# Kernel optimization log

Measured on AMD Instinct MI355X. Metric: run time of the kernel, lower is better.

The kernel has to match this reference:

```python
import jax, jax.numpy as jnp
import numpy as np

B, N, D = 64, 2048, 128  # batch, neighbors, embedding_dim (= region_dim)


def setup_inputs() -> dict:
    key = jax.random.key(0)
    ks = jax.random.split(key, 8)
    inv_sqrt_d = 1.0 / np.sqrt(D).astype(np.float32)
    return {
        "e_i": jax.random.normal(ks[0], (B, D), jnp.float32),
        "e_j": jax.random.normal(ks[1], (B, N, D), jnp.float32),
        "imp_j": jax.random.uniform(ks[2], (B, N), jnp.float32),
        "R_lk": jax.random.normal(ks[3], (D, D), jnp.float32),
        "W_q": jax.random.normal(ks[4], (D, D), jnp.float32) * inv_sqrt_d,
        "W_k": jax.random.normal(ks[5], (D, D), jnp.float32) * inv_sqrt_d,
        "W_v": jax.random.normal(ks[6], (D, D), jnp.float32) * inv_sqrt_d,
        "omega": jax.random.normal(ks[7], (D,), jnp.float32),
    }


def reference(e_i, e_j, imp_j, R_lk, W_q, W_k, W_v, omega):
    # torch nn.Linear(x) = x @ W.T; weights are [out, in] = [D, D]
    q = e_i @ W_q.T                                   # [B, D]
    k = jnp.einsum('bnd,ed->bne', e_j, W_k)           # [B, N, D]
    # additive tanh attention score sigma_ij = tanh(q_i + k_j) . omega
    sigma = jnp.tanh(q[:, None, :] + k) @ omega       # [B, N]
    exp_s = jnp.exp(sigma)
    denom = jnp.sum(exp_s, axis=1, keepdims=True) + 1e-9
    a = imp_j * exp_s / denom                         # [B, N]  (a_ij, squeezed)
    v = jnp.einsum('bnd,ed->bne', e_j, W_v)           # [B, N, D]
    # A_i_t = sum_n a_ij * v_j  (identical math to A_i_l in the source)
    A_l = jnp.einsum('bn,bnd->bd', a, v)              # [B, D]
    # sum_n R[l,k] * a[b,n] * v[b,n,k] = R[l,k] * A_l[b,k]  -- fused, no [B,N,D,D]
    A_lk = R_lk[None, :, :] * A_l[:, None, :]         # [B, D, D]
    return A_l, A_lk, A_l
```

## Files before the change

kernel.cpp:

```cpp
#include <hip/hip_runtime.h>
#include <stdint.h>

#define BB 64
#define NN 2048
#define DD 128
#define ROWS 64
#define CPB 2

typedef __attribute__((ext_vector_type(8))) short short8;
typedef __attribute__((ext_vector_type(4))) float f32x4;

__device__ __forceinline__ unsigned short f2bf_rtne(float x) {
    union { float f; unsigned int u; } v; v.f = x;
    unsigned int r = v.u + 0x7fffu + ((v.u >> 16) & 1u);
    return (unsigned short)(r >> 16);
}
__device__ __forceinline__ float bf2f(unsigned short h) {
    union { unsigned int u; float f; } v; v.u = ((unsigned int)h) << 16;
    return v.f;
}
__device__ __forceinline__ float tanh_fast(float x) {
    float ax = fabsf(x);
    float e  = __expf(-2.f * ax);
    float t  = (1.f - e) / (1.f + e);
    return copysignf(t, x);
}

__global__ __launch_bounds__(256) void aegis_prep(
    const float* __restrict__ e_i, const float* __restrict__ Wq,
    const float* __restrict__ Wk,
    float* __restrict__ qbuf, unsigned short* __restrict__ Bhig,
    unsigned short* __restrict__ Blog,
    float* __restrict__ sprime, float* __restrict__ denom)
{
    __shared__ float eis[DD];
    const int t = threadIdx.x, blk = blockIdx.x;
    if (blk < 8) {
        const int tid = blk * 256 + t;
        const int lr = tid & 15, lg = (tid >> 4) & 3, ks = (tid >> 6) & 3, et = tid >> 8;
        const int e = et * 16 + lr, k = ks * 32 + lg * 8;
        const float* src = Wk + e * DD + k;
        float4 x0 = *reinterpret_cast<const float4*>(src);
        float4 x1 = *reinterpret_cast<const float4*>(src + 4);
        float xs[8] = {x0.x, x0.y, x0.z, x0.w, x1.x, x1.y, x1.z, x1.w};
        short8 h, l;
        #pragma unroll
        for (int j = 0; j < 8; ++j) {
            unsigned short hb = f2bf_rtne(xs[j]);
            float rem = xs[j] - bf2f(hb);
            h[j] = (short)hb;
            l[j] = (short)f2bf_rtne(rem);
        }
        *reinterpret_cast<short8*>(Bhig + (size_t)tid * 8) = h;
        *reinterpret_cast<short8*>(Blog + (size_t)tid * 8) = l;
    } else {
        const int b = blk - 8;
        if (t < DD) eis[t] = e_i[b * DD + t];
        __syncthreads();
        if (t < DD) {
            float acc = 0.f;
            const float4* wr = reinterpret_cast<const float4*>(Wq + t * DD);
            const float4* ev = reinterpret_cast<const float4*>(eis);
            #pragma unroll 8
            for (int i = 0; i < 32; ++i) {
                float4 w = wr[i], e = ev[i];
                acc = fmaf(w.x, e.x, acc); acc = fmaf(w.y, e.y, acc);
                acc = fmaf(w.z, e.z, acc); acc = fmaf(w.w, e.w, acc);
            }
            qbuf[b * DD + t] = acc;
            sprime[b * DD + t] = 0.f;
        }
        if (t == 0) denom[b] = 0.f;
    }
}

__global__ __launch_bounds__(256, 4) void aegis_main(
    const float* __restrict__ e_j, const float* __restrict__ imp,
    const float* __restrict__ omega, const float* __restrict__ qbuf,
    const unsigned short* __restrict__ Bhig, const unsigned short* __restrict__ Blog,
    float* __restrict__ sprime, float* __restrict__ denom)
{
    __shared__ unsigned short Ehi[ROWS * DD];
    __shared__ unsigned short Elo[ROWS * DD];
    __shared__ float sig[ROWS][4];
    __shared__ float wrow[ROWS];
    __shared__ float scol[DD];

    const int t    = threadIdx.x;
    const int b    = blockIdx.x >> 4;
    const int cb   = blockIdx.x & 15;
    const int lane = t & 63;
    const int w    = t >> 6;
    const int lr   = lane & 15;
    const int lg   = lane >> 4;

    short8 Bh[2][4], Bl[2][4];
    #pragma unroll
    for (int ct = 0; ct < 2; ++ct)
        #pragma unroll
        for (int ks = 0; ks < 4; ++ks) {
            const int fi = (((2 * w + ct) * 4 + ks) * 4 + lg) * 16 + lr;
            Bh[ct][ks] = *reinterpret_cast<const short8*>(Bhig + (size_t)fi * 8);
            Bl[ct][ks] = *reinterpret_cast<const short8*>(Blog + (size_t)fi * 8);
        }

    float qv[2], ov[2];
    #pragma unroll
    for (int ct = 0; ct < 2; ++ct) {
        const int c = 32 * w + 16 * ct + lr;
        qv[ct] = qbuf[b * DD + c];
        ov[ct] = omega[c];
    }

    const int d  = t & 127;
    const int hf = t >> 7;
    float sacc = 0.f, den_local = 0.f;

    #pragma unroll 1
    for (int c = 0; c < CPB; ++c) {
        const int row0 = (cb * CPB + c) * ROWS;
        __syncthreads();

        {
            const float4* src = reinterpret_cast<const float4*>(
                e_j + ((size_t)(b * NN + row0)) * DD);
            #pragma unroll
            for (int i = 0; i < 8; ++i) {
                const int idx = t + i * 256;
                const int rr  = idx >> 5;
                const int bc  = (idx & 31) * 8;
                float4 v = src[idx];
                float xs[4] = {v.x, v.y, v.z, v.w};
                unsigned short hs[4], ls[4];
                #pragma unroll
                for (int j = 0; j < 4; ++j) {
                    hs[j] = f2bf_rtne(xs[j]);
                    ls[j] = f2bf_rtne(xs[j] - bf2f(hs[j]));
                }
                uint2 ph, pl;
                ph.x = (unsigned)hs[0] | ((unsigned)hs[1] << 16);
                ph.y = (unsigned)hs[2] | ((unsigned)hs[3] << 16);
                pl.x = (unsigned)ls[0] | ((unsigned)ls[1] << 16);
                pl.y = (unsigned)ls[2] | ((unsigned)ls[3] << 16);
                const int off = rr * 256 + (bc ^ ((rr & 7) << 4));
                *reinterpret_cast<uint2*>(reinterpret_cast<char*>(Ehi) + off) = ph;
                *reinterpret_cast<uint2*>(reinterpret_cast<char*>(Elo) + off) = pl;
            }
        }
        __syncthreads();

        #pragma unroll 1
        for (int rt = 0; rt < 4; ++rt) {
            f32x4 a0 = {0.f, 0.f, 0.f, 0.f};
            f32x4 a1 = {0.f, 0.f, 0.f, 0.f};
            const int arow = rt * 16 + lr;
            const int rbase = arow * 256;
            const int rsw   = (lr & 7) << 4;
            #pragma unroll
            for (int ks = 0; ks < 4; ++ks) {
                const int off = rbase + ((ks * 64 + lg * 16) ^ rsw);
                short8 ah = *reinterpret_cast<const short8*>(
                    reinterpret_cast<const char*>(Ehi) + off);
                short8 al = *reinterpret_cast<const short8*>(
                    reinterpret_cast<const char*>(Elo) + off);
                a0 = __builtin_amdgcn_mfma_f32_16x16x32_bf16(ah, Bh[0][ks], a0, 0, 0, 0);
                a1 = __builtin_amdgcn_mfma_f32_16x16x32_bf16(ah, Bh[1][ks], a1, 0, 0, 0);
                a0 = __builtin_amdgcn_mfma_f32_16x16x32_bf16(ah, Bl[0][ks], a0, 0, 0, 0);
                a1 = __builtin_amdgcn_mfma_f32_16x16x32_bf16(ah, Bl[1][ks], a1, 0, 0, 0);
                a0 = __builtin_amdgcn_mfma_f32_16x16x32_bf16(al, Bh[0][ks], a0, 0, 0, 0);
                a1 = __builtin_amdgcn_mfma_f32_16x16x32_bf16(al, Bh[1][ks], a1, 0, 0, 0);
            }
            float sp[4];
            #pragma unroll
            for (int i = 0; i < 4; ++i) {
                float x0 = qv[0] + a0[i];
                float x1 = qv[1] + a1[i];
                sp[i] = fmaf(ov[0], tanh_fast(x0), ov[1] * tanh_fast(x1));
            }
            #pragma unroll
            for (int m = 1; m < 16; m <<= 1) {
                #pragma unroll
                for (int i = 0; i < 4; ++i) sp[i] += __shfl_xor(sp[i], m);
            }
            if (lr == 0) {
                #pragma unroll
                for (int i = 0; i < 4; ++i) sig[rt * 16 + 4 * lg + i][w] = sp[i];
            }
        }
        __syncthreads();

        if (t < ROWS) {
            float sg = sig[t][0] + sig[t][1] + sig[t][2] + sig[t][3];
            float es = __expf(sg);
            wrow[t]  = es * imp[b * NN + row0 + t];
            float ds = es;
            #pragma unroll
            for (int m = 1; m < 64; m <<= 1) ds += __shfl_xor(ds, m);
            if (t == 0) den_local += ds;
        }
        __syncthreads();

        {
            float part = 0.f;
            #pragma unroll
            for (int rr = hf * 32; rr < hf * 32 + 32; ++rr) {
                const int off = rr * 256 + ((2 * d) ^ ((rr & 7) << 4));
                float ev = bf2f(*reinterpret_cast<const unsigned short*>(
                               reinterpret_cast<const char*>(Ehi) + off))
                         + bf2f(*reinterpret_cast<const unsigned short*>(
                               reinterpret_cast<const char*>(Elo) + off));
                part = fmaf(wrow[rr], ev, part);
            }
            sacc += part;
        }
    }

    if (hf == 0) scol[d] = sacc;
    __syncthreads();
    if (hf == 1) atomicAdd(&sprime[b * DD + d], sacc + scol[d]);
    if (t == 0) atomicAdd(&denom[b], den_local);
}

__global__ __launch_bounds__(256) void aegis_epi(
    const float* __restrict__ sprime, const float* __restrict__ denomv,
    const float* __restrict__ Wv, const float* __restrict__ R,
    float* __restrict__ out)
{
    __shared__ float sn[DD];
    __shared__ float alred[DD][2];
    __shared__ float al[DD];
    const int t = threadIdx.x, b = blockIdx.x;

    if (t < DD) sn[t] = sprime[b * DD + t] / (denomv[b] + 1e-9f);
    __syncthreads();
    {
        const int l = t >> 1, h = t & 1;
        const float4* wr = reinterpret_cast<const float4*>(Wv + l * DD + h * 64);
        const float4* sv = reinterpret_cast<const float4*>(sn + h * 64);
        float acc = 0.f;
        #pragma unroll 8
        for (int i = 0; i < 16; ++i) {
            float4 w = wr[i], e = sv[i];
            acc = fmaf(w.x, e.x, acc); acc = fmaf(w.y, e.y, acc);
            acc = fmaf(w.z, e.z, acc); acc = fmaf(w.w, e.w, acc);
        }
        alred[l][h] = acc;
    }
    __syncthreads();
    if (t < DD) {
        float v = alred[t][0] + alred[t][1];
        al[t] = v;
        out[b * DD + t] = v;
        out[8192 + 1048576 + b * DD + t] = v;
    }
    __syncthreads();
    float4* dst = reinterpret_cast<float4*>(out + 8192 + (size_t)b * DD * DD);
    const float4* rsrc = reinterpret_cast<const float4*>(R);
    #pragma unroll
    for (int i = 0; i < 16; ++i) {
        const int idx = t + i * 256;
        float4 r = rsrc[idx];
        const int k0 = (idx & 31) * 4;
        float4 o;
        o.x = r.x * al[k0];     o.y = r.y * al[k0 + 1];
        o.z = r.z * al[k0 + 2]; o.w = r.w * al[k0 + 3];
        dst[idx] = o;
    }
}

extern "C" void kernel_launch(void* const* d_in, const int* in_sizes, int n_in,
                              void* d_out, int out_size, void* d_ws, size_t ws_size,
                              hipStream_t stream) {
    const float* e_i = (const float*)d_in[0];
    const float* e_j = (const float*)d_in[1];
    const float* imp = (const float*)d_in[2];
    const float* R   = (const float*)d_in[3];
    const float* Wq  = (const float*)d_in[4];
    const float* Wk  = (const float*)d_in[5];
    const float* Wv  = (const float*)d_in[6];
    const float* om  = (const float*)d_in[7];

    float* out    = (float*)d_out;
    float* sprime = (float*)d_ws;
    float* denom  = (float*)((char*)d_ws + 32768);

    float* qbuf = out + 8192;
    unsigned short* Bhig = (unsigned short*)(out + 8192 + 8192);
    unsigned short* Blog = Bhig + 16384;

    aegis_prep<<<dim3(72), dim3(256), 0, stream>>>(
        e_i, Wq, Wk, qbuf, Bhig, Blog, sprime, denom);
    aegis_main<<<dim3(BB * 16), dim3(256), 0, stream>>>(
        e_j, imp, om, qbuf, Bhig, Blog, sprime, denom);
    aegis_epi<<<dim3(BB), dim3(256), 0, stream>>>(sprime, denom, Wv, R, out);
}
```

Before: 159.4 us.

## Prefetch next e_j chunk into registers and restructure weighted-sum reduction in main kernel

The main kernel now loads both 64-row chunks of e_j into registers up front. The second chunk's global load is issued before the first chunk's MFMA score phase, so the memory latency overlaps compute. The weighted column sum is reworked so each thread reads packed pairs of bf16 values across 16 rows and partial sums are combined through shared memory. Barriers become a custom LDS-wait plus s_barrier. Occupancy is lowered from 4 to 3 blocks per CU to make room for the extra registers held by the prefetch buffer.

```diff
diff --git a/kernel.cpp b/kernel.cpp
--- a/kernel.cpp
+++ b/kernel.cpp
@@ -24,6 +24,10 @@
     float e  = __expf(-2.f * ax);
     float t  = (1.f - e) / (1.f + e);
     return copysignf(t, x);
+}
+__device__ __forceinline__ void ldsbar() {
+    asm volatile("s_waitcnt lgkmcnt(0)" ::: "memory");
+    __builtin_amdgcn_s_barrier();
 }
 
 __global__ __launch_bounds__(256) void aegis_prep(
@@ -74,7 +78,7 @@
     }
 }
 
-__global__ __launch_bounds__(256, 4) void aegis_main(
+__global__ __launch_bounds__(256, 3) void aegis_main(
     const float* __restrict__ e_j, const float* __restrict__ imp,
     const float* __restrict__ omega, const float* __restrict__ qbuf,
     const unsigned short* __restrict__ Bhig, const unsigned short* __restrict__ Blog,
@@ -84,7 +88,7 @@
     __shared__ unsigned short Elo[ROWS * DD];
     __shared__ float sig[ROWS][4];
     __shared__ float wrow[ROWS];
-    __shared__ float scol[DD];
+    __shared__ float scolq[4][DD];
 
     const int t    = threadIdx.x;
     const int b    = blockIdx.x >> 4;
@@ -93,6 +97,13 @@
     const int w    = t >> 6;
     const int lr   = lane & 15;
     const int lg   = lane >> 4;
+    const int row0 = cb * (CPB * ROWS);
+
+    float4 st[8];
+    const float4* ejp = reinterpret_cast<const float4*>(
+        e_j + (size_t)(b * NN + row0) * DD);
+    #pragma unroll
+    for (int i = 0; i < 8; ++i) st[i] = ejp[t + i * 256];
 
     short8 Bh[2][4], Bl[2][4];
     #pragma unroll
@@ -111,26 +122,125 @@
         qv[ct] = qbuf[b * DD + c];
         ov[ct] = omega[c];
     }
-
-    const int d  = t & 127;
-    const int hf = t >> 7;
+    float impv[CPB];
+    if (t < ROWS) {
+        #pragma unroll
+        for (int c = 0; c < CPB; ++c) impv[c] = imp[b * NN + row0 + c * ROWS + t];
+    }
+
+    #pragma unroll
+    for (int i = 0; i < 8; ++i) {
+        const int idx = t + i * 256;
+        const int rr  = idx >> 5;
+        const int bc  = (idx & 31) * 8;
+        float xs[4] = {st[i].x, st[i].y, st[i].z, st[i].w};
+        unsigned short hs[4], ls[4];
+        #pragma unroll
+        for (int j = 0; j < 4; ++j) {
+            hs[j] = f2bf_rtne(xs[j]);
+            ls[j] = f2bf_rtne(xs[j] - bf2f(hs[j]));
+        }
+        uint2 ph, pl;
+        ph.x = (unsigned)hs[0] | ((unsigned)hs[1] << 16);
+        ph.y = (unsigned)hs[2] | ((unsigned)hs[3] << 16);
+        pl.x = (unsigned)ls[0] | ((unsigned)ls[1] << 16);
+        pl.y = (unsigned)ls[2] | ((unsigned)ls[3] << 16);
+        const int off = rr * 256 + (bc ^ ((rr & 7) << 4));
+        *reinterpret_cast<uint2*>(reinterpret_cast<char*>(Ehi) + off) = ph;
+        *reinterpret_cast<uint2*>(reinterpret_cast<char*>(Elo) + off) = pl;
+    }
+    #pragma unroll
+    for (int i = 0; i < 8; ++i) st[i] = ejp[2048 + t + i * 256];
+
+    ldsbar();
+
     float sacc = 0.f, den_local = 0.f;
-
-    #pragma unroll 1
+    const int rq = t >> 6;
+    const int cp = t & 63;
+
+    #pragma unroll
     for (int c = 0; c < CPB; ++c) {
-        const int row0 = (cb * CPB + c) * ROWS;
-        __syncthreads();
+        #pragma unroll 1
+        for (int rt = 0; rt < 4; ++rt) {
+            f32x4 a0 = {0.f, 0.f, 0.f, 0.f};
+            f32x4 a1 = {0.f, 0.f, 0.f, 0.f};
+            const int arow  = rt * 16 + lr;
+            const int rbase = arow * 256;
+            const int rsw   = (lr & 7) << 4;
+            #pragma unroll
+            for (int ks = 0; ks < 4; ++ks) {
+                const int off = rbase + ((ks * 64 + lg * 16) ^ rsw);
+                short8 ah = *reinterpret_cast<const short8*>(
+                    reinterpret_cast<const char*>(Ehi) + off);
+                short8 al = *reinterpret_cast<const short8*>(
+                    reinterpret_cast<const char*>(Elo) + off);
+                a0 = __builtin_amdgcn_mfma_f32_16x16x32_bf16(ah, Bh[0][ks], a0, 0, 0, 0);
+                a1 = __builtin_amdgcn_mfma_f32_16x16x32_bf16(ah, Bh[1][ks], a1, 0, 0, 0);
+                a0 = __builtin_amdgcn_mfma_f32_16x16x32_bf16(ah, Bl[0][ks], a0, 0, 0, 0);
+                a1 = __builtin_amdgcn_mfma_f32_16x16x32_bf16(ah, Bl[1][ks], a1, 0, 0, 0);
+                a0 = __builtin_amdgcn_mfma_f32_16x16x32_bf16(al, Bh[0][ks], a0, 0, 0, 0);
+                a1 = __builtin_amdgcn_mfma_f32_16x16x32_bf16(al, Bh[1][ks], a1, 0, 0, 0);
+            }
+            float sp[4];
+            #pragma unroll
+            for (int i = 0; i < 4; ++i) {
+                float x0 = qv[0] + a0[i];
+                float x1 = qv[1] + a1[i];
+                sp[i] = fmaf(ov[0], tanh_fast(x0), ov[1] * tanh_fast(x1));
+            }
+            #pragma unroll
+            for (int m = 1; m < 16; m <<= 1) {
+                #pragma unroll
+                for (int i = 0; i < 4; ++i) sp[i] += __shfl_xor(sp[i], m);
+            }
+            if (lr == 0) {
+                #pragma unroll
+                for (int i = 0; i < 4; ++i) sig[rt * 16 + 4 * lg + i][w] = sp[i];
+            }
+        }
+        ldsbar();
+
+        if (t < ROWS) {
+            float sg = sig[t][0] + sig[t][1] + sig[t][2] + sig[t][3];
+            float es = __expf(sg);
+            wrow[t]  = es * impv[c];
+            float ds = es;
+            #pragma unroll
+            for (int m = 1; m < 64; m <<= 1) ds += __shfl_xor(ds, m);
+            if (t == 0) den_local += ds;
+        }
+        ldsbar();
 
         {
-            const float4* src = reinterpret_cast<const float4*>(
-                e_j + ((size_t)(b * NN + row0)) * DD);
+            float a0 = 0.f, a1 = 0.f;
+            #pragma unroll
+            for (int j = 0; j < 16; ++j) {
+                const int rr  = rq * 16 + j;
+                const int off = rr * 256 + ((4 * cp) ^ ((rr & 7) << 4));
+                const unsigned hbits = *reinterpret_cast<const unsigned*>(
+                    reinterpret_cast<const char*>(Ehi) + off);
+                const unsigned lbits = *reinterpret_cast<const unsigned*>(
+                    reinterpret_cast<const char*>(Elo) + off);
+                const float wv = wrow[rr];
+                float v0 = bf2f((unsigned short)hbits) + bf2f((unsigned short)lbits);
+                float v1 = bf2f((unsigned short)(hbits >> 16)) + bf2f((unsigned short)(lbits >> 16));
+                a0 = fmaf(wv, v0, a0);
+                a1 = fmaf(wv, v1, a1);
+            }
+            scolq[rq][2 * cp]     = a0;
+            scolq[rq][2 * cp + 1] = a1;
+        }
+        ldsbar();
+
+        if (t < DD) sacc += scolq[0][t] + scolq[1][t] + scolq[2][t] + scolq[3][t];
+
+        if (c + 1 < CPB) {
             #pragma unroll
             for (int i = 0; i < 8; ++i) {
                 const int idx = t + i * 256;
                 const int rr  = idx >> 5;
                 const int bc  = (idx & 31) * 8;
-                float4 v = src[idx];
-                float xs[4] = {v.x, v.y, v.z, v.w};
+                float xs[4] = {st[i].x, st[i].y, st[i].z, st[i].w};
                 unsigned short hs[4], ls[4];
                 #pragma unroll
                 for (int j = 0; j < 4; ++j) {
@@ -146,78 +256,11 @@
                 *reinterpret_cast<uint2*>(reinterpret_cast<char*>(Ehi) + off) = ph;
                 *reinterpret_cast<uint2*>(reinterpret_cast<char*>(Elo) + off) = pl;
             }
-        }
-        __syncthreads();
-
-        #pragma unroll 1
-        for (int rt = 0; rt < 4; ++rt) {
-            f32x4 a0 = {0.f, 0.f, 0.f, 0.f};
-            f32x4 a1 = {0.f, 0.f, 0.f, 0.f};
-            const int arow = rt * 16 + lr;
-            const int rbase = arow * 256;
-            const int rsw   = (lr & 7) << 4;
-            #pragma unroll
-            for (int ks = 0; ks < 4; ++ks) {
-                const int off = rbase + ((ks * 64 + lg * 16) ^ rsw);
-                short8 ah = *reinterpret_cast<const short8*>(
-                    reinterpret_cast<const char*>(Ehi) + off);
-                short8 al = *reinterpret_cast<const short8*>(
-                    reinterpret_cast<const char*>(Elo) + off);
-                a0 = __builtin_amdgcn_mfma_f32_16x16x32_bf16(ah, Bh[0][ks], a0, 0, 0, 0);
-                a1 = __builtin_amdgcn_mfma_f32_16x16x32_bf16(ah, Bh[1][ks], a1, 0, 0, 0);
-                a0 = __builtin_amdgcn_mfma_f32_16x16x32_bf16(ah, Bl[0][ks], a0, 0, 0, 0);
-                a1 = __builtin_amdgcn_mfma_f32_16x16x32_bf16(ah, Bl[1][ks], a1, 0, 0, 0);
-                a0 = __builtin_amdgcn_mfma_f32_16x16x32_bf16(al, Bh[0][ks], a0, 0, 0, 0);
-                a1 = __builtin_amdgcn_mfma_f32_16x16x32_bf16(al, Bh[1][ks], a1, 0, 0, 0);
-            }
-            float sp[4];
-            #pragma unroll
-            for (int i = 0; i < 4; ++i) {
-                float x0 = qv[0] + a0[i];
-                float x1 = qv[1] + a1[i];
-                sp[i] = fmaf(ov[0], tanh_fast(x0), ov[1] * tanh_fast(x1));
-            }
-            #pragma unroll
-            for (int m = 1; m < 16; m <<= 1) {
-                #pragma unroll
-                for (int i = 0; i < 4; ++i) sp[i] += __shfl_xor(sp[i], m);
-            }
-            if (lr == 0) {
-                #pragma unroll
-                for (int i = 0; i < 4; ++i) sig[rt * 16 + 4 * lg + i][w] = sp[i];
-            }
-        }
-        __syncthreads();
-
-        if (t < ROWS) {
-            float sg = sig[t][0] + sig[t][1] + sig[t][2] + sig[t][3];
-            float es = __expf(sg);
-            wrow[t]  = es * imp[b * NN + row0 + t];
-            float ds = es;
-            #pragma unroll
-            for (int m = 1; m < 64; m <<= 1) ds += __shfl_xor(ds, m);
-            if (t == 0) den_local += ds;
-        }
-        __syncthreads();
-
-        {
-            float part = 0.f;
-            #pragma unroll
-            for (int rr = hf * 32; rr < hf * 32 + 32; ++rr) {
-                const int off = rr * 256 + ((2 * d) ^ ((rr & 7) << 4));
-                float ev = bf2f(*reinterpret_cast<const unsigned short*>(
-                               reinterpret_cast<const char*>(Ehi) + off))
-                         + bf2f(*reinterpret_cast<const unsigned short*>(
-                               reinterpret_cast<const char*>(Elo) + off));
-                part = fmaf(wrow[rr], ev, part);
-            }
-            sacc += part;
-        }
-    }
-
-    if (hf == 0) scol[d] = sacc;
-    __syncthreads();
-    if (hf == 1) atomicAdd(&sprime[b * DD + d], sacc + scol[d]);
+            ldsbar();
+        }
+    }
+
+    if (t < DD) atomicAdd(&sprime[b * DD + t], sacc);
     if (t == 0) atomicAdd(&denom[b], den_local);
 }
 
```

Result: faster. 153.3 us (-3.8%).
